# Performance work log

Measured on AMD Instinct MI355X. Metric: run time of the kernel, lower is better.

## Reference

```python
import jax, jax.numpy as jnp
import numpy as np

DIM = 512

def setup_inputs() -> dict:
    key = jax.random.key(0)
    kx, kq, kk, kv = jax.random.split(key, 4)
    x = jax.random.normal(kx, (8, 2048, DIM), dtype=jnp.float32)
    # Dense kernels are [in_dim, out_dim], no bias
    Wq = jax.random.normal(kq, (DIM, DIM), dtype=jnp.float32) * (DIM ** -0.5)
    Wk = jax.random.normal(kk, (DIM, DIM), dtype=jnp.float32) * (DIM ** -0.5)
    Wv = jax.random.normal(kv, (DIM, DIM), dtype=jnp.float32) * (DIM ** -0.5)
    return {"x": x, "Wq": Wq, "Wk": Wk, "Wv": Wv}

def reference(x, Wq, Wk, Wv):
    # x: [b, s, d]
    q = jnp.einsum('bsd,de->bse', x, Wq)
    k = jnp.einsum('bsd,de->bse', x, Wk)
    v = jnp.einsum('bsd,de->bse', x, Wv)
    scale = jnp.sqrt(jnp.asarray(DIM, dtype=x.dtype))
    attn = jnp.einsum('bqe,bke->bqk', q, k) / scale  # [b, s, s]
    attn = jax.nn.softmax(attn, axis=-1)
    return jnp.einsum('bqk,bke->bqe', attn, v)  # [b, s, d]
```

## Files before the change

### kernel.cpp

```cpp
#include <hip/hip_runtime.h>
#include <stdint.h>

typedef unsigned short u16;
typedef unsigned int u32;
typedef float floatx4 __attribute__((ext_vector_type(4)));
typedef __bf16 bf16x8 __attribute__((ext_vector_type(8)));
typedef __attribute__((address_space(1))) const u32 gu32;
typedef __attribute__((address_space(3))) u32 lu32;

#define SEQ 2048
#define DIM 512
#define NBATCH 8

#if defined(__has_builtin)
#if __has_builtin(__builtin_amdgcn_cvt_pk_bf16_f32)
#define HAVE_PK_BF16 1
#endif
#endif
#ifndef HAVE_PK_BF16
#define HAVE_PK_BF16 0
#endif

__device__ __forceinline__ u16 f2bf(float f) {
#if HAVE_PK_BF16
  auto p = __builtin_amdgcn_cvt_pk_bf16_f32(f, f);
  union { decltype(p) v; u16 u[2]; } cv; cv.v = p;
  return cv.u[0];
#else
  u32 u = __float_as_uint(f);
  u += 0x7fffu + ((u >> 16) & 1u);
  return (u16)(u >> 16);
#endif
}

__device__ __forceinline__ void stage_tile64(const u16* __restrict__ g, int ld, int k0, u16* lds) {
  const int t = threadIdx.x;
  const int wave = t >> 6, lane = t & 63;
  const int rsub = lane >> 3;
  const int lg = (lane & 7) ^ rsub;
#pragma unroll
  for (int q = 0; q < 4; ++q) {
    const int chunk = wave * 4 + q;
    const int row = chunk * 8 + rsub;
    const u16* gp = g + (size_t)row * ld + k0 + lg * 8;
    u16* lp = lds + chunk * 512 + lane * 8;
    __builtin_amdgcn_global_load_lds((gu32*)gp, (lu32*)lp, 16, 0, 0);
  }
}

__device__ __forceinline__ void gemm_core(const u16* A, const u16* BT, int lda, int ldb, int kdim,
                                          u16* As, u16* Bs, floatx4 acc[4][4]) {
  const int t = threadIdx.x;
  const int wave = t >> 6, lane = t & 63;
  const int wr = (wave >> 1) * 64, wc = (wave & 1) * 64;
  const int l15 = lane & 15, quad = lane >> 4;
  const int swz = l15 & 7;
  for (int k0 = 0; k0 < kdim; k0 += 64) {
    stage_tile64(A, lda, k0, As);
    stage_tile64(BT, ldb, k0, Bs);
    __syncthreads();
#pragma unroll
    for (int ks = 0; ks < 2; ++ks) {
      const int pg = ((ks << 2) + quad) ^ swz;
      bf16x8 af[4], bfr[4];
#pragma unroll
      for (int i = 0; i < 4; ++i) {
        af[i]  = *(const bf16x8*)(As + (wr + i * 16 + l15) * 64 + pg * 8);
        bfr[i] = *(const bf16x8*)(Bs + (wc + i * 16 + l15) * 64 + pg * 8);
      }
#pragma unroll
      for (int mi = 0; mi < 4; ++mi)
#pragma unroll
        for (int ni = 0; ni < 4; ++ni)
          acc[mi][ni] = __builtin_amdgcn_mfma_f32_16x16x32_bf16(af[mi], bfr[ni], acc[mi][ni], 0, 0, 0);
    }
    __syncthreads();
  }
}

__device__ __forceinline__ void zero_acc(floatx4 acc[4][4]) {
#pragma unroll
  for (int i = 0; i < 4; ++i)
#pragma unroll
    for (int j = 0; j < 4; ++j)
      acc[i][j] = (floatx4){0.f, 0.f, 0.f, 0.f};
}

__global__ __launch_bounds__(256) void k_prep(const float* __restrict__ x,
                                              const float* __restrict__ Wq, const float* __restrict__ Wk,
                                              const float* __restrict__ Wv,
                                              u16* __restrict__ xb, u16* __restrict__ wt) {
  __shared__ float tile[64][65];
  const int t = threadIdx.x;
  if (blockIdx.x < 4096) {
    size_t i = ((size_t)blockIdx.x * 256 + t) * 8;
    float4 a = *(const float4*)(x + i);
    float4 b = *(const float4*)(x + i + 4);
    u16 o[8] = {f2bf(a.x), f2bf(a.y), f2bf(a.z), f2bf(a.w),
                f2bf(b.x), f2bf(b.y), f2bf(b.z), f2bf(b.w)};
    *(uint4*)(xb + i) = *(const uint4*)o;
    return;
  }
  const int r = blockIdx.x - 4096;
  const int sec = r >> 6, rem = r & 63;
  const int kb = (rem & 7) * 64, nb0 = (rem >> 3) * 64;
  const float* W = (sec == 0) ? Wq : (sec == 1) ? Wk : Wv;
#pragma unroll
  for (int i = 0; i < 4; ++i) {
    int kr = i * 16 + (t >> 4), nc = (t & 15) * 4;
    float4 v = *(const float4*)&W[(size_t)(kb + kr) * 512 + nb0 + nc];
    tile[kr][nc] = v.x; tile[kr][nc + 1] = v.y; tile[kr][nc + 2] = v.z; tile[kr][nc + 3] = v.w;
  }
  __syncthreads();
#pragma unroll
  for (int i = 0; i < 4; ++i) {
    int nr = i * 16 + (t >> 4), kc = (t & 15) * 4;
    u16 o[4] = {f2bf(tile[kc][nr]), f2bf(tile[kc + 1][nr]), f2bf(tile[kc + 2][nr]), f2bf(tile[kc + 3][nr])};
    *(uint2*)&wt[(size_t)(sec * 512 + nb0 + nr) * 512 + kb + kc] = *(const uint2*)o;
  }
}

__global__ __launch_bounds__(256, 4) void k_qkv(const u16* __restrict__ xb, const u16* __restrict__ wt,
                                                u16* __restrict__ qo, u16* __restrict__ ko,
                                                u16* __restrict__ vt) {
  __shared__ __align__(16) u16 As[128 * 64];
  __shared__ __align__(16) u16 Bs[128 * 64];
  const int m0 = blockIdx.x * 128, n0 = blockIdx.y * 128;
  floatx4 acc[4][4];
  zero_acc(acc);
  gemm_core(xb + (size_t)m0 * DIM, wt + (size_t)n0 * DIM, DIM, DIM, DIM, As, Bs, acc);
  const int t = threadIdx.x, wave = t >> 6, lane = t & 63;
  const int wr = (wave >> 1) * 64, wc = (wave & 1) * 64;
  const int l15 = lane & 15, quad = lane >> 4;
  const int sec = n0 >> 9;
#pragma unroll
  for (int mi = 0; mi < 4; ++mi)
#pragma unroll
    for (int ni = 0; ni < 4; ++ni)
#pragma unroll
      for (int r = 0; r < 4; ++r) {
        int m = m0 + wr + mi * 16 + quad * 4 + r;
        int n = n0 + wc + ni * 16 + l15;
        float v = acc[mi][ni][r];
        int nc = n & 511;
        if (sec == 0) {
          qo[(size_t)m * DIM + nc] = f2bf(v * 0.04419417382415922f);
        } else if (sec == 1) {
          ko[(size_t)m * DIM + nc] = f2bf(v);
        } else {
          int b = m >> 11, s = m & 2047;
          vt[((size_t)(b * DIM + nc)) * SEQ + s] = f2bf(v);
        }
      }
}

__global__ __launch_bounds__(256, 4) void k_scores(const u16* __restrict__ q, const u16* __restrict__ kk,
                                                   u16* __restrict__ sc, float* __restrict__ rowsum,
                                                   int b0) {
  __shared__ __align__(16) u16 As[128 * 64];
  __shared__ __align__(16) u16 Bs[128 * 64];
  const int bz = blockIdx.z, bb = b0 + bz;
  const int xcd = blockIdx.x & 7, j = blockIdx.x >> 3;
  const int m0 = (j & 15) * 128, n0 = (xcd * 2 + (j >> 4)) * 128;
  floatx4 acc[4][4];
  zero_acc(acc);
  gemm_core(q + (size_t)bb * SEQ * DIM + (size_t)m0 * DIM,
            kk + (size_t)bb * SEQ * DIM + (size_t)n0 * DIM, DIM, DIM, DIM, As, Bs, acc);
  u16* C = sc + (size_t)bz * SEQ * SEQ;
  float* rsb = rowsum + (size_t)bb * SEQ;
  const int t = threadIdx.x, wave = t >> 6, lane = t & 63;
  const int wr = (wave >> 1) * 64, wc = (wave & 1) * 64;
  const int l15 = lane & 15, quad = lane >> 4;
#pragma unroll
  for (int mi = 0; mi < 4; ++mi)
#pragma unroll
    for (int r = 0; r < 4; ++r) {
      int m = m0 + wr + mi * 16 + quad * 4 + r;
      float p = 0.f;
      float ev[4];
#pragma unroll
      for (int ni = 0; ni < 4; ++ni) {
        ev[ni] = __expf(acc[mi][ni][r]);
        p += ev[ni];
      }
#pragma unroll
      for (int ni = 0; ni < 4; ++ni) {
        int n = n0 + wc + ni * 16 + l15;
        C[(size_t)m * SEQ + n] = f2bf(ev[ni]);
      }
      p += __shfl_xor(p, 1); p += __shfl_xor(p, 2);
      p += __shfl_xor(p, 4); p += __shfl_xor(p, 8);
      if (l15 == 0) atomicAdd(&rsb[m], p);
    }
}

__global__ __launch_bounds__(256, 4) void k_pv(const u16* __restrict__ sc, const u16* __restrict__ vt,
                                               const float* __restrict__ rowsum,
                                               float* __restrict__ out, int b0) {
  __shared__ __align__(16) u16 As[128 * 64];
  __shared__ __align__(16) u16 Bs[128 * 64];
  const int bz = blockIdx.z, bb = b0 + bz;
  const int xcd = blockIdx.x & 7, j = blockIdx.x >> 3;
  const int m0 = (xcd * 2 + (j & 1)) * 128, n0 = (j >> 1) * 128;
  floatx4 acc[4][4];
  zero_acc(acc);
  gemm_core(sc + (size_t)bz * SEQ * SEQ + (size_t)m0 * SEQ,
            vt + (size_t)bb * DIM * SEQ + (size_t)n0 * SEQ, SEQ, SEQ, SEQ, As, Bs, acc);
  float* C = out + (size_t)bb * SEQ * DIM;
  const float* rsb = rowsum + (size_t)bb * SEQ;
  const int t = threadIdx.x, wave = t >> 6, lane = t & 63;
  const int wr = (wave >> 1) * 64, wc = (wave & 1) * 64;
  const int l15 = lane & 15, quad = lane >> 4;
#pragma unroll
  for (int mi = 0; mi < 4; ++mi)
#pragma unroll
    for (int r = 0; r < 4; ++r) {
      int m = m0 + wr + mi * 16 + quad * 4 + r;
      float inv = 1.0f / rsb[m];
#pragma unroll
      for (int ni = 0; ni < 4; ++ni) {
        int n = n0 + wc + ni * 16 + l15;
        C[(size_t)m * DIM + n] = acc[mi][ni][r] * inv;
      }
    }
}

extern "C" void kernel_launch(void* const* d_in, const int* in_sizes, int n_in,
                              void* d_out, int out_size, void* d_ws, size_t ws_size,
                              hipStream_t stream) {
  const float* x  = (const float*)d_in[0];
  const float* Wq = (const float*)d_in[1];
  const float* Wk = (const float*)d_in[2];
  const float* Wv = (const float*)d_in[3];
  float* out = (float*)d_out;
  char* ws = (char*)d_ws;

  u16* xb   = (u16*)(ws + 0);
  u16* wt   = (u16*)(ws + 16777216);
  u16* qo   = (u16*)(ws + 18350080);
  u16* ko   = (u16*)(ws + 35127296);
  u16* vt   = (u16*)(ws + 51904512);
  float* rs = (float*)(ws + 68681728);
  u16* sc   = (u16*)(ws + 68747264);
  const size_t base_need = 68747264;
  const size_t per_b = (size_t)SEQ * SEQ * 2;
  size_t avail = (ws_size > base_need) ? (ws_size - base_need) : 0;
  int nb = (int)(avail / per_b);
  if (nb < 1) nb = 1;
  if (nb > NBATCH) nb = NBATCH;

  hipMemsetAsync(rs, 0, (size_t)NBATCH * SEQ * sizeof(float), stream);
  k_prep<<<dim3(4288), dim3(256), 0, stream>>>(x, Wq, Wk, Wv, xb, wt);
  k_qkv<<<dim3(128, 12), dim3(256), 0, stream>>>(xb, wt, qo, ko, vt);
  for (int b0 = 0; b0 < NBATCH; b0 += nb) {
    int nbr = (NBATCH - b0 < nb) ? (NBATCH - b0) : nb;
    k_scores<<<dim3(256, 1, nbr), dim3(256), 0, stream>>>(qo, ko, sc, rs, b0);
    k_pv<<<dim3(64, 1, nbr), dim3(256), 0, stream>>>(sc, vt, rs, out, b0);
  }
}
```

Baseline: 216.0 us.

## Fuse scores and PV into flash-style attention kernel, drop LDS staging in QKV

Replaces the separate scores and PV GEMM kernels, which round-trip the full SxS probability matrix through global memory and use atomics for row sums, with one fused kernel. That kernel computes QK^T per key block, exponentiates into a double-buffered LDS tile, and accumulates P·V in registers, normalizing at the end. The QKV projection now reads operands straight from global memory instead of LDS staging, and the packed bf16 conversion builtin is removed. The fused kernel launches only 256 blocks of 512 threads and reloads Q/K/V fragments directly from global memory each iteration, which may leave it short on occupancy and more bound on memory latency.

```diff
diff --git a/kernel.cpp b/kernel.cpp
--- a/kernel.cpp
+++ b/kernel.cpp
@@ -5,85 +5,16 @@
 typedef unsigned int u32;
 typedef float floatx4 __attribute__((ext_vector_type(4)));
 typedef __bf16 bf16x8 __attribute__((ext_vector_type(8)));
-typedef __attribute__((address_space(1))) const u32 gu32;
-typedef __attribute__((address_space(3))) u32 lu32;
 
 #define SEQ 2048
 #define DIM 512
 #define NBATCH 8
-
-#if defined(__has_builtin)
-#if __has_builtin(__builtin_amdgcn_cvt_pk_bf16_f32)
-#define HAVE_PK_BF16 1
-#endif
-#endif
-#ifndef HAVE_PK_BF16
-#define HAVE_PK_BF16 0
-#endif
+#define PS 136
 
 __device__ __forceinline__ u16 f2bf(float f) {
-#if HAVE_PK_BF16
-  auto p = __builtin_amdgcn_cvt_pk_bf16_f32(f, f);
-  union { decltype(p) v; u16 u[2]; } cv; cv.v = p;
-  return cv.u[0];
-#else
   u32 u = __float_as_uint(f);
   u += 0x7fffu + ((u >> 16) & 1u);
   return (u16)(u >> 16);
-#endif
-}
-
-__device__ __forceinline__ void stage_tile64(const u16* __restrict__ g, int ld, int k0, u16* lds) {
-  const int t = threadIdx.x;
-  const int wave = t >> 6, lane = t & 63;
-  const int rsub = lane >> 3;
-  const int lg = (lane & 7) ^ rsub;
-#pragma unroll
-  for (int q = 0; q < 4; ++q) {
-    const int chunk = wave * 4 + q;
-    const int row = chunk * 8 + rsub;
-    const u16* gp = g + (size_t)row * ld + k0 + lg * 8;
-    u16* lp = lds + chunk * 512 + lane * 8;
-    __builtin_amdgcn_global_load_lds((gu32*)gp, (lu32*)lp, 16, 0, 0);
-  }
-}
-
-__device__ __forceinline__ void gemm_core(const u16* A, const u16* BT, int lda, int ldb, int kdim,
-                                          u16* As, u16* Bs, floatx4 acc[4][4]) {
-  const int t = threadIdx.x;
-  const int wave = t >> 6, lane = t & 63;
-  const int wr = (wave >> 1) * 64, wc = (wave & 1) * 64;
-  const int l15 = lane & 15, quad = lane >> 4;
-  const int swz = l15 & 7;
-  for (int k0 = 0; k0 < kdim; k0 += 64) {
-    stage_tile64(A, lda, k0, As);
-    stage_tile64(BT, ldb, k0, Bs);
-    __syncthreads();
-#pragma unroll
-    for (int ks = 0; ks < 2; ++ks) {
-      const int pg = ((ks << 2) + quad) ^ swz;
-      bf16x8 af[4], bfr[4];
-#pragma unroll
-      for (int i = 0; i < 4; ++i) {
-        af[i]  = *(const bf16x8*)(As + (wr + i * 16 + l15) * 64 + pg * 8);
-        bfr[i] = *(const bf16x8*)(Bs + (wc + i * 16 + l15) * 64 + pg * 8);
-      }
-#pragma unroll
-      for (int mi = 0; mi < 4; ++mi)
-#pragma unroll
-        for (int ni = 0; ni < 4; ++ni)
-          acc[mi][ni] = __builtin_amdgcn_mfma_f32_16x16x32_bf16(af[mi], bfr[ni], acc[mi][ni], 0, 0, 0);
-    }
-    __syncthreads();
-  }
-}
-
-__device__ __forceinline__ void zero_acc(floatx4 acc[4][4]) {
-#pragma unroll
-  for (int i = 0; i < 4; ++i)
-#pragma unroll
-    for (int j = 0; j < 4; ++j)
-      acc[i][j] = (floatx4){0.f, 0.f, 0.f, 0.f};
 }
 
 __global__ __launch_bounds__(256) void k_prep(const float* __restrict__ x,
@@ -120,18 +51,42 @@
   }
 }
 
-__global__ __launch_bounds__(256, 4) void k_qkv(const u16* __restrict__ xb, const u16* __restrict__ wt,
+__global__ __launch_bounds__(256, 3) void k_qkv(const u16* __restrict__ xb, const u16* __restrict__ wt,
                                                 u16* __restrict__ qo, u16* __restrict__ ko,
                                                 u16* __restrict__ vt) {
-  __shared__ __align__(16) u16 As[128 * 64];
-  __shared__ __align__(16) u16 Bs[128 * 64];
-  const int m0 = blockIdx.x * 128, n0 = blockIdx.y * 128;
-  floatx4 acc[4][4];
-  zero_acc(acc);
-  gemm_core(xb + (size_t)m0 * DIM, wt + (size_t)n0 * DIM, DIM, DIM, DIM, As, Bs, acc);
   const int t = threadIdx.x, wave = t >> 6, lane = t & 63;
   const int wr = (wave >> 1) * 64, wc = (wave & 1) * 64;
   const int l15 = lane & 15, quad = lane >> 4;
+  const int m0 = blockIdx.x * 128, n0 = blockIdx.y * 128;
+
+  floatx4 acc[4][4];
+#pragma unroll
+  for (int i = 0; i < 4; ++i)
+#pragma unroll
+    for (int j = 0; j < 4; ++j)
+      acc[i][j] = (floatx4){0.f, 0.f, 0.f, 0.f};
+
+  const u16* Arow[4];
+  const u16* Brow[4];
+#pragma unroll
+  for (int i = 0; i < 4; ++i) {
+    Arow[i] = xb + (size_t)(m0 + wr + i * 16 + l15) * DIM + quad * 8;
+    Brow[i] = wt + (size_t)(n0 + wc + i * 16 + l15) * DIM + quad * 8;
+  }
+#pragma unroll
+  for (int kc = 0; kc < 16; ++kc) {
+    bf16x8 a[4], b[4];
+#pragma unroll
+    for (int i = 0; i < 4; ++i) a[i] = *(const bf16x8*)(Arow[i] + kc * 32);
+#pragma unroll
+    for (int i = 0; i < 4; ++i) b[i] = *(const bf16x8*)(Brow[i] + kc * 32);
+#pragma unroll
+    for (int mi = 0; mi < 4; ++mi)
+#pragma unroll
+      for (int ni = 0; ni < 4; ++ni)
+        acc[mi][ni] = __builtin_amdgcn_mfma_f32_16x16x32_bf16(a[mi], b[ni], acc[mi][ni], 0, 0, 0);
+  }
+
   const int sec = n0 >> 9;
 #pragma unroll
   for (int mi = 0; mi < 4; ++mi)
@@ -154,75 +109,114 @@
       }
 }
 
-__global__ __launch_bounds__(256, 4) void k_scores(const u16* __restrict__ q, const u16* __restrict__ kk,
-                                                   u16* __restrict__ sc, float* __restrict__ rowsum,
-                                                   int b0) {
-  __shared__ __align__(16) u16 As[128 * 64];
-  __shared__ __align__(16) u16 Bs[128 * 64];
-  const int bz = blockIdx.z, bb = b0 + bz;
-  const int xcd = blockIdx.x & 7, j = blockIdx.x >> 3;
-  const int m0 = (j & 15) * 128, n0 = (xcd * 2 + (j >> 4)) * 128;
-  floatx4 acc[4][4];
-  zero_acc(acc);
-  gemm_core(q + (size_t)bb * SEQ * DIM + (size_t)m0 * DIM,
-            kk + (size_t)bb * SEQ * DIM + (size_t)n0 * DIM, DIM, DIM, DIM, As, Bs, acc);
-  u16* C = sc + (size_t)bz * SEQ * SEQ;
-  float* rsb = rowsum + (size_t)bb * SEQ;
-  const int t = threadIdx.x, wave = t >> 6, lane = t & 63;
-  const int wr = (wave >> 1) * 64, wc = (wave & 1) * 64;
+__global__ __launch_bounds__(512, 2) void k_att(const u16* __restrict__ qo, const u16* __restrict__ ko,
+                                                const u16* __restrict__ vt, float* __restrict__ out) {
+  __shared__ __align__(16) u16 P[2][64 * PS];
+  __shared__ float RS[4][64];
+  const int t = threadIdx.x, w = t >> 6, lane = t & 63;
   const int l15 = lane & 15, quad = lane >> 4;
-#pragma unroll
-  for (int mi = 0; mi < 4; ++mi)
-#pragma unroll
-    for (int r = 0; r < 4; ++r) {
-      int m = m0 + wr + mi * 16 + quad * 4 + r;
-      float p = 0.f;
-      float ev[4];
-#pragma unroll
-      for (int ni = 0; ni < 4; ++ni) {
-        ev[ni] = __expf(acc[mi][ni][r]);
-        p += ev[ni];
-      }
-#pragma unroll
-      for (int ni = 0; ni < 4; ++ni) {
-        int n = n0 + wc + ni * 16 + l15;
-        C[(size_t)m * SEQ + n] = f2bf(ev[ni]);
-      }
-      p += __shfl_xor(p, 1); p += __shfl_xor(p, 2);
-      p += __shfl_xor(p, 4); p += __shfl_xor(p, 8);
-      if (l15 == 0) atomicAdd(&rsb[m], p);
+  const int wm = w & 1, wd = w >> 1;
+  const int bx = blockIdx.x, b = bx & 7, m0 = (bx >> 3) * 64;
+  const u16* Qb = qo + (size_t)b * SEQ * DIM;
+  const u16* Kb = ko + (size_t)b * SEQ * DIM;
+  const u16* Vb = vt + (size_t)b * DIM * SEQ;
+  float* Ob = out + (size_t)b * SEQ * DIM;
+
+  const u16* qrow[2];
+  const u16* vrow[8];
+#pragma unroll
+  for (int i = 0; i < 2; ++i)
+    qrow[i] = Qb + (size_t)(m0 + wm * 32 + i * 16 + l15) * DIM + quad * 8;
+#pragma unroll
+  for (int i = 0; i < 8; ++i)
+    vrow[i] = Vb + (size_t)(wd * 128 + i * 16 + l15) * SEQ + quad * 8;
+
+  floatx4 O[2][8];
+#pragma unroll
+  for (int i = 0; i < 2; ++i)
+#pragma unroll
+    for (int j = 0; j < 8; ++j)
+      O[i][j] = (floatx4){0.f, 0.f, 0.f, 0.f};
+  floatx4 rsum[2] = {(floatx4){0.f, 0.f, 0.f, 0.f}, (floatx4){0.f, 0.f, 0.f, 0.f}};
+
+  for (int j = 0; j < 16; ++j) {
+    floatx4 s[2][2];
+#pragma unroll
+    for (int a = 0; a < 2; ++a)
+#pragma unroll
+      for (int c = 0; c < 2; ++c)
+        s[a][c] = (floatx4){0.f, 0.f, 0.f, 0.f};
+    const u16* krow[2];
+#pragma unroll
+    for (int i = 0; i < 2; ++i)
+      krow[i] = Kb + (size_t)(j * 128 + wd * 32 + i * 16 + l15) * DIM + quad * 8;
+#pragma unroll
+    for (int kc = 0; kc < 16; ++kc) {
+      bf16x8 aq[2], bk[2];
+      aq[0] = *(const bf16x8*)(qrow[0] + kc * 32);
+      aq[1] = *(const bf16x8*)(qrow[1] + kc * 32);
+      bk[0] = *(const bf16x8*)(krow[0] + kc * 32);
+      bk[1] = *(const bf16x8*)(krow[1] + kc * 32);
+#pragma unroll
+      for (int ms = 0; ms < 2; ++ms)
+#pragma unroll
+        for (int ns = 0; ns < 2; ++ns)
+          s[ms][ns] = __builtin_amdgcn_mfma_f32_16x16x32_bf16(aq[ms], bk[ns], s[ms][ns], 0, 0, 0);
     }
-}
-
-__global__ __launch_bounds__(256, 4) void k_pv(const u16* __restrict__ sc, const u16* __restrict__ vt,
-                                               const float* __restrict__ rowsum,
-                                               float* __restrict__ out, int b0) {
-  __shared__ __align__(16) u16 As[128 * 64];
-  __shared__ __align__(16) u16 Bs[128 * 64];
-  const int bz = blockIdx.z, bb = b0 + bz;
-  const int xcd = blockIdx.x & 7, j = blockIdx.x >> 3;
-  const int m0 = (xcd * 2 + (j & 1)) * 128, n0 = (j >> 1) * 128;
-  floatx4 acc[4][4];
-  zero_acc(acc);
-  gemm_core(sc + (size_t)bz * SEQ * SEQ + (size_t)m0 * SEQ,
-            vt + (size_t)bb * DIM * SEQ + (size_t)n0 * SEQ, SEQ, SEQ, SEQ, As, Bs, acc);
-  float* C = out + (size_t)bb * SEQ * DIM;
-  const float* rsb = rowsum + (size_t)bb * SEQ;
-  const int t = threadIdx.x, wave = t >> 6, lane = t & 63;
-  const int wr = (wave >> 1) * 64, wc = (wave & 1) * 64;
-  const int l15 = lane & 15, quad = lane >> 4;
-#pragma unroll
-  for (int mi = 0; mi < 4; ++mi)
-#pragma unroll
-    for (int r = 0; r < 4; ++r) {
-      int m = m0 + wr + mi * 16 + quad * 4 + r;
-      float inv = 1.0f / rsb[m];
-#pragma unroll
-      for (int ni = 0; ni < 4; ++ni) {
-        int n = n0 + wc + ni * 16 + l15;
-        C[(size_t)m * DIM + n] = acc[mi][ni][r] * inv;
-      }
+    u16* Pb = (u16*)P[j & 1];
+#pragma unroll
+    for (int ms = 0; ms < 2; ++ms)
+#pragma unroll
+      for (int ns = 0; ns < 2; ++ns)
+#pragma unroll
+        for (int r = 0; r < 4; ++r) {
+          float e = __expf(s[ms][ns][r]);
+          rsum[ms][r] += e;
+          Pb[(wm * 32 + ms * 16 + quad * 4 + r) * PS + wd * 32 + ns * 16 + l15] = f2bf(e);
+        }
+    asm volatile("s_waitcnt lgkmcnt(0)\ns_barrier" ::: "memory");
+#pragma unroll
+    for (int kc = 0; kc < 4; ++kc) {
+      bf16x8 ap[2], bv[8];
+      ap[0] = *(const bf16x8*)(Pb + (wm * 32 + l15) * PS + kc * 32 + quad * 8);
+      ap[1] = *(const bf16x8*)(Pb + (wm * 32 + 16 + l15) * PS + kc * 32 + quad * 8);
+#pragma unroll
+      for (int ds = 0; ds < 8; ++ds)
+        bv[ds] = *(const bf16x8*)(vrow[ds] + j * 128 + kc * 32);
+#pragma unroll
+      for (int ms = 0; ms < 2; ++ms)
+#pragma unroll
+        for (int ds = 0; ds < 8; ++ds)
+          O[ms][ds] = __builtin_amdgcn_mfma_f32_16x16x32_bf16(ap[ms], bv[ds], O[ms][ds], 0, 0, 0);
     }
+  }
+
+#pragma unroll
+  for (int ms = 0; ms < 2; ++ms) {
+    floatx4 rs = rsum[ms];
+#pragma unroll
+    for (int off = 1; off < 16; off <<= 1) {
+      rs[0] += __shfl_xor(rs[0], off);
+      rs[1] += __shfl_xor(rs[1], off);
+      rs[2] += __shfl_xor(rs[2], off);
+      rs[3] += __shfl_xor(rs[3], off);
+    }
+    if (l15 == 0) *(floatx4*)&RS[wd][wm * 32 + ms * 16 + quad * 4] = rs;
+  }
+  __syncthreads();
+#pragma unroll
+  for (int ms = 0; ms < 2; ++ms) {
+    const int row = wm * 32 + ms * 16 + quad * 4;
+    floatx4 inv;
+#pragma unroll
+    for (int r = 0; r < 4; ++r)
+      inv[r] = 1.0f / (RS[0][row + r] + RS[1][row + r] + RS[2][row + r] + RS[3][row + r]);
+#pragma unroll
+    for (int ds = 0; ds < 8; ++ds)
+#pragma unroll
+      for (int r = 0; r < 4; ++r)
+        Ob[(size_t)(m0 + row + r) * DIM + wd * 128 + ds * 16 + l15] = O[ms][ds][r] * inv[r];
+  }
 }
 
 extern "C" void kernel_launch(void* const* d_in, const int* in_sizes, int n_in,
@@ -235,26 +229,13 @@
   float* out = (float*)d_out;
   char* ws = (char*)d_ws;
 
-  u16* xb   = (u16*)(ws + 0);
-  u16* wt   = (u16*)(ws + 16777216);
-  u16* qo   = (u16*)(ws + 18350080);
-  u16* ko   = (u16*)(ws + 35127296);
-  u16* vt   = (u16*)(ws + 51904512);
-  float* rs = (float*)(ws + 68681728);
-  u16* sc   = (u16*)(ws + 68747264);
-  const size_t base_need = 68747264;
-  const size_t per_b = (size_t)SEQ * SEQ * 2;
-  size_t avail = (ws_size > base_need) ? (ws_size - base_need) : 0;
-  int nb = (int)(avail / per_b);
-  if (nb < 1) nb = 1;
-  if (nb > NBATCH) nb = NBATCH;
-
-  hipMemsetAsync(rs, 0, (size_t)NBATCH * SEQ * sizeof(float), stream);
+  u16* xb = (u16*)(ws + 0);
+  u16* wt = (u16*)(ws + 16777216);
+  u16* qo = (u16*)(ws + 18350080);
+  u16* ko = (u16*)(ws + 35127296);
+  u16* vt = (u16*)(ws + 51904512);
+
   k_prep<<<dim3(4288), dim3(256), 0, stream>>>(x, Wq, Wk, Wv, xb, wt);
   k_qkv<<<dim3(128, 12), dim3(256), 0, stream>>>(xb, wt, qo, ko, vt);
-  for (int b0 = 0; b0 < NBATCH; b0 += nb) {
-    int nbr = (NBATCH - b0 < nb) ? (NBATCH - b0) : nb;
-    k_scores<<<dim3(256, 1, nbr), dim3(256), 0, stream>>>(qo, ko, sc, rs, b0);
-    k_pv<<<dim3(64, 1, nbr), dim3(256), 0, stream>>>(sc, vt, rs, out, b0);
-  }
-}
+  k_att<<<dim3(256), dim3(512), 0, stream>>>(qo, ko, vt, out);
+}
```

Measured after the change: 444.0 us. 2.06x slower.
